# Kernel tuning notes

Measured on AMD Instinct MI355X. Metric: run time of the kernel, lower is better.

Reference implementation:

```python
import jax, jax.numpy as jnp
import numpy as np
import math

VOCAB = 50257
BLOCK = 2048
NE = 768


def setup_inputs() -> dict:
    key = jax.random.key(0)
    ks = jax.random.split(key, 12)
    s = 0.02
    idx = jax.random.randint(ks[0], (4, 2048), 0, VOCAB, dtype=jnp.int64 if jax.config.jax_enable_x64 else jnp.int32)
    tok_emb = jax.random.normal(ks[1], (VOCAB, NE), jnp.float32) * s
    pos_emb = jax.random.normal(ks[2], (BLOCK, NE), jnp.float32) * s
    Wk = jax.random.normal(ks[3], (NE, NE), jnp.float32) * s
    bk = jnp.zeros((NE,), jnp.float32)
    Wq = jax.random.normal(ks[4], (NE, NE), jnp.float32) * s
    bq = jnp.zeros((NE,), jnp.float32)
    Wv = jax.random.normal(ks[5], (NE, NE), jnp.float32) * s
    bv = jnp.zeros((NE,), jnp.float32)
    ln_g = jnp.ones((NE,), jnp.float32)
    ln_b = jnp.zeros((NE,), jnp.float32)
    Wh = jax.random.normal(ks[6], (NE, VOCAB), jnp.float32) * s
    bh = jnp.zeros((VOCAB,), jnp.float32)
    return {"idx": idx, "tok_emb": tok_emb, "pos_emb": pos_emb, "Wq": Wq, "bq": bq,
            "Wk": Wk, "bk": bk, "Wv": Wv, "bv": bv, "ln_g": ln_g, "ln_b": ln_b,
            "Wh": Wh, "bh": bh}


def reference(idx, tok_emb, pos_emb, Wq, bq, Wk, bk, Wv, bv, ln_g, ln_b, Wh, bh):
    B, T = idx.shape
    C = tok_emb.shape[1]
    x = tok_emb[idx] + pos_emb[:T]  # [B,T,C]
    q = jnp.einsum('btc,cd->btd', x, Wq) + bq
    k = jnp.einsum('btc,cd->btd', x, Wk) + bk
    v = jnp.einsum('btc,cd->btd', x, Wv) + bv
    att = jnp.einsum('btd,bsd->bts', q, k) / math.sqrt(C)  # [B,T,T]
    causal = jnp.tril(jnp.ones((T, T), bool))
    att = jnp.where(causal, att, -jnp.inf)
    att = jax.nn.softmax(att, axis=-1)
    y = jnp.einsum('bts,bsd->btd', att, v)
    # LayerNorm (eps=1e-5, torch default)
    mu = jnp.mean(y, axis=-1, keepdims=True)
    var = jnp.mean((y - mu) ** 2, axis=-1, keepdims=True)
    yn = (y - mu) * jax.lax.rsqrt(var + 1e-5) * ln_g + ln_b
    logits = jnp.einsum('btc,cv->btv', yn, Wh) + bh
    return logits
```

## Files before the change

### kernel.cpp

```cpp
#include <hip/hip_runtime.h>
#include <hip/hip_bf16.h>
#include <math.h>

typedef __bf16 bf16x8 __attribute__((ext_vector_type(8)));
typedef float  f32x4  __attribute__((ext_vector_type(4)));

#define GAS(p) ((const __attribute__((address_space(1))) void*)(p))
#define LAS(p) ((__attribute__((address_space(3))) void*)(p))

static constexpr int NE = 768;

__global__ __launch_bounds__(256) void k_embed(const int* __restrict__ idx,
    const float* __restrict__ tok, const float* __restrict__ pos,
    __hip_bfloat16* __restrict__ xb)
{
    int bt = blockIdx.x;
    int t  = bt & 2047;
    int token = idx[bt];
    const float* te = tok + (size_t)token * NE;
    const float* pe = pos + (size_t)t * NE;
    __hip_bfloat16* o = xb + (size_t)bt * NE;
    for (int c = threadIdx.x; c < NE; c += 256)
        o[c] = __float2bfloat16(te[c] + pe[c]);
}

__global__ __launch_bounds__(256) void k_transpose_f32_bf16(
    const float* __restrict__ in, __hip_bfloat16* __restrict__ out,
    int R, int C, int outRows)
{
    __shared__ float tile[32][33];
    int c0 = blockIdx.x * 32, r0 = blockIdx.y * 32;
    int tx = threadIdx.x & 31, ty = threadIdx.x >> 5;
    #pragma unroll
    for (int i = 0; i < 32; i += 8) {
        int r = r0 + ty + i, c = c0 + tx;
        tile[ty + i][tx] = (r < R && c < C) ? in[(size_t)r * C + c] : 0.f;
    }
    __syncthreads();
    #pragma unroll
    for (int i = 0; i < 32; i += 8) {
        int oc = c0 + ty + i, orr = r0 + tx;
        if (oc < outRows && orr < R)
            out[(size_t)oc * R + orr] = __float2bfloat16(tile[tx][ty + i]);
    }
}

__global__ __launch_bounds__(256) void k_transpose_bf16(
    const __hip_bfloat16* __restrict__ in, __hip_bfloat16* __restrict__ out,
    int R, int C)
{
    __shared__ __hip_bfloat16 tile[32][33];
    size_t boff = (size_t)blockIdx.z * R * C;
    int c0 = blockIdx.x * 32, r0 = blockIdx.y * 32;
    int tx = threadIdx.x & 31, ty = threadIdx.x >> 5;
    #pragma unroll
    for (int i = 0; i < 32; i += 8)
        tile[ty + i][tx] = in[boff + (size_t)(r0 + ty + i) * C + (c0 + tx)];
    __syncthreads();
    #pragma unroll
    for (int i = 0; i < 32; i += 8)
        out[boff + (size_t)(c0 + ty + i) * R + (r0 + tx)] = tile[tx][ty + i];
}

__global__ __launch_bounds__(256) void k_pack_bias(const float* __restrict__ bq,
    const float* __restrict__ bk, const float* __restrict__ bv, float* __restrict__ o)
{
    int i = blockIdx.x * 256 + threadIdx.x;
    if (i < 768) o[i] = bq[i];
    else if (i < 1536) o[i] = bk[i - 768];
    else if (i < 2304) o[i] = bv[i - 1536];
}

template<int MODE>
__global__ __launch_bounds__(256) void k_gemm(
    const __hip_bfloat16* __restrict__ A, const __hip_bfloat16* __restrict__ Bt,
    int K, int lda, int ldb,
    size_t strideA, size_t strideB, size_t strideC,
    float* __restrict__ outf, int ldc, int ncols,
    const float* __restrict__ bias, float scale,
    __hip_bfloat16* __restrict__ oq, __hip_bfloat16* __restrict__ ok,
    __hip_bfloat16* __restrict__ ov)
{
    int bn = blockIdx.x, bm = blockIdx.y, bz = blockIdx.z;
    if constexpr (MODE == 2) bm = (int)gridDim.y - 1 - bm;
    if (MODE == 1 && bn > bm) return;
    __shared__ __align__(16) __hip_bfloat16 As[128 * 32];
    __shared__ __align__(16) __hip_bfloat16 Bs[128 * 32];
    const __hip_bfloat16* Ab = A  + bz * strideA + (size_t)bm * 128 * lda;
    const __hip_bfloat16* Bb = Bt + bz * strideB + (size_t)bn * 128 * ldb;
    int tid = threadIdx.x, w = tid >> 6, lane = tid & 63;
    int wr = w >> 1, wc = w & 1;
    f32x4 acc[4][4] = {};
    int sr = tid >> 2, sc = (tid & 3) * 8;
    int lr = lane & 15, lk = (lane >> 4) * 8;

    const int kend = (MODE == 2) ? (bm + 1) * 128 : K;

    for (int k0 = 0; k0 < kend; k0 += 32) {
        __syncthreads();
        #pragma unroll
        for (int i = 0; i < 2; ++i) {
            __builtin_amdgcn_global_load_lds(GAS(Ab + (size_t)(i * 64 + sr) * lda + k0 + sc),
                                             LAS((char*)As + i * 4096 + w * 1024), 16, 0, 0);
            __builtin_amdgcn_global_load_lds(GAS(Bb + (size_t)(i * 64 + sr) * ldb + k0 + sc),
                                             LAS((char*)Bs + i * 4096 + w * 1024), 16, 0, 0);
        }
        __syncthreads();
        bf16x8 af[4], bfv[4];
        #pragma unroll
        for (int mi = 0; mi < 4; ++mi)
            af[mi] = *(const bf16x8*)(As + (wr * 64 + mi * 16 + lr) * 32 + lk);
        #pragma unroll
        for (int ni = 0; ni < 4; ++ni)
            bfv[ni] = *(const bf16x8*)(Bs + (wc * 64 + ni * 16 + lr) * 32 + lk);
        #pragma unroll
        for (int mi = 0; mi < 4; ++mi)
            #pragma unroll
            for (int ni = 0; ni < 4; ++ni)
                acc[mi][ni] = __builtin_amdgcn_mfma_f32_16x16x32_bf16(af[mi], bfv[ni], acc[mi][ni], 0, 0, 0);
    }

    int r4 = (lane >> 4) * 4;
    #pragma unroll
    for (int mi = 0; mi < 4; ++mi) {
        #pragma unroll
        for (int ni = 0; ni < 4; ++ni) {
            #pragma unroll
            for (int r = 0; r < 4; ++r) {
                int row = bm * 128 + wr * 64 + mi * 16 + r4 + r;
                int col = bn * 128 + wc * 64 + ni * 16 + lr;
                float v = acc[mi][ni][r];
                if constexpr (MODE == 0) {
                    v += bias[col];
                    __hip_bfloat16 h = __float2bfloat16(v);
                    if (col < 768)       oq[(size_t)row * 768 + col]          = h;
                    else if (col < 1536) ok[(size_t)row * 768 + (col - 768)]  = h;
                    else                 ov[(size_t)row * 768 + (col - 1536)] = h;
                } else if constexpr (MODE == 1) {
                    outf[bz * strideC + (size_t)row * ldc + col] = v * scale;
                } else {
                    outf[bz * strideC + (size_t)row * ldc + col] = v;
                }
            }
        }
    }
}

__global__ __launch_bounds__(512, 4) void k_gemm_head(
    const __hip_bfloat16* __restrict__ A,
    const __hip_bfloat16* __restrict__ Bt,
    float* __restrict__ out, const float* __restrict__ bias, int ldc, int ncols)
{
    constexpr int K = 768, NT = K / 32;
    __shared__ __align__(16) __hip_bfloat16 As[2][256 * 32];
    __shared__ __align__(16) __hip_bfloat16 Bs[2][128 * 32];

    const int bm = blockIdx.x, bn = blockIdx.y;
    const int tid = threadIdx.x;
    const int w = tid >> 6, lane = tid & 63;
    const int wr = w >> 1, wc = w & 1;
    const int lr = lane & 15, lu = lane >> 4;

    const __hip_bfloat16* Ap = A  + (size_t)(bm * 256) * K;
    const __hip_bfloat16* Bp = Bt + (size_t)(bn * 128) * K;

    f32x4 acc[4][4] = {};

    auto stage = [&](int kt, int pb) {
        #pragma unroll
        for (int l = 0; l < 2; ++l) {
            int v = l * 512 + tid;
            int row = v >> 2, uc = v & 3;
            int s = (row >> 1) & 3;
            __builtin_amdgcn_global_load_lds(GAS(Ap + (size_t)row * K + kt * 32 + ((uc ^ s) << 3)),
                                             LAS(&As[pb][v * 8]), 16, 0, 0);
        }
        {
            int v = tid;
            int row = v >> 2, uc = v & 3;
            int s = (row >> 1) & 3;
            __builtin_amdgcn_global_load_lds(GAS(Bp + (size_t)row * K + kt * 32 + ((uc ^ s) << 3)),
                                             LAS(&Bs[pb][v * 8]), 16, 0, 0);
        }
    };
    auto rdA = [&](int pb, int m) {
        int row = wr * 64 + m * 16 + lr;
        int s = (row >> 1) & 3;
        return *(const bf16x8*)&As[pb][row * 32 + ((lu ^ s) << 3)];
    };
    auto rdB = [&](int pb, int n) {
        int row = wc * 64 + n * 16 + lr;
        int s = (row >> 1) & 3;
        return *(const bf16x8*)&Bs[pb][row * 32 + ((lu ^ s) << 3)];
    };

    stage(0, 0);
    __syncthreads();

    for (int kt = 0; kt < NT; ++kt) {
        const int p = kt & 1;
        if (kt + 1 < NT) stage(kt + 1, p ^ 1);
        bf16x8 bfv[4];
        #pragma unroll
        for (int n = 0; n < 4; ++n) bfv[n] = rdB(p, n);
        #pragma unroll
        for (int m = 0; m < 4; ++m) {
            bf16x8 a = rdA(p, m);
            #pragma unroll
            for (int n = 0; n < 4; ++n)
                acc[m][n] = __builtin_amdgcn_mfma_f32_16x16x32_bf16(a, bfv[n], acc[m][n], 0, 0, 0);
        }
        __syncthreads();
    }

    const int r4 = lu * 4;
    #pragma unroll
    for (int m = 0; m < 4; ++m) {
        #pragma unroll
        for (int n = 0; n < 4; ++n) {
            int col = bn * 128 + wc * 64 + n * 16 + lr;
            if (col < ncols) {
                float bv_ = bias[col];
                #pragma unroll
                for (int r = 0; r < 4; ++r) {
                    int row = bm * 256 + wr * 64 + m * 16 + r4 + r;
                    out[(size_t)row * ldc + col] = acc[m][n][r] + bv_;
                }
            }
        }
    }
}

__global__ __launch_bounds__(256) void k_softmax(const float* __restrict__ att,
    __hip_bfloat16* __restrict__ P, int T)
{
    int t = blockIdx.x, b = blockIdx.y;
    const float* row = att + ((size_t)b * T + t) * T;
    __hip_bfloat16* prow = P + ((size_t)b * T + t) * T;
    const int n = t + 1;
    const int nz = ((t >> 7) + 1) << 7;
    __shared__ float red[256];
    float4 v[2];
    float mx = -1e30f;
    #pragma unroll
    for (int j = 0; j < 2; ++j) {
        int e = (threadIdx.x + j * 256) * 4;
        v[j] = *(const float4*)(row + e);
        #pragma unroll
        for (int k = 0; k < 4; ++k)
            if (e + k < n) mx = fmaxf(mx, ((const float*)&v[j])[k]);
    }
    red[threadIdx.x] = mx; __syncthreads();
    for (int o = 128; o > 0; o >>= 1) {
        if (threadIdx.x < o) red[threadIdx.x] = fmaxf(red[threadIdx.x], red[threadIdx.x + o]);
        __syncthreads();
    }
    mx = red[0]; __syncthreads();
    float ev[8];
    float sum = 0.f;
    #pragma unroll
    for (int j = 0; j < 2; ++j) {
        int e = (threadIdx.x + j * 256) * 4;
        #pragma unroll
        for (int k = 0; k < 4; ++k) {
            float x = ((const float*)&v[j])[k];
            float ex = (e + k < n) ? __expf(x - mx) : 0.f;
            ev[j * 4 + k] = ex;
            sum += ex;
        }
    }
    red[threadIdx.x] = sum; __syncthreads();
    for (int o = 128; o > 0; o >>= 1) {
        if (threadIdx.x < o) red[threadIdx.x] += red[threadIdx.x + o];
        __syncthreads();
    }
    float inv = 1.f / red[0];
    #pragma unroll
    for (int j = 0; j < 2; ++j) {
        int e = (threadIdx.x + j * 256) * 4;
        #pragma unroll
        for (int k = 0; k < 4; ++k)
            if (e + k < nz) prow[e + k] = __float2bfloat16(ev[j * 4 + k] * inv);
    }
}

__global__ __launch_bounds__(256) void k_layernorm(const float* __restrict__ y,
    const float* __restrict__ g, const float* __restrict__ b,
    __hip_bfloat16* __restrict__ yn)
{
    int row = blockIdx.x;
    const float* yr = y + (size_t)row * NE;
    float s = 0.f, s2 = 0.f;
    for (int c = threadIdx.x; c < NE; c += 256) { float v = yr[c]; s += v; s2 += v * v; }
    __shared__ float r1[256], r2[256];
    r1[threadIdx.x] = s; r2[threadIdx.x] = s2; __syncthreads();
    for (int o = 128; o > 0; o >>= 1) {
        if (threadIdx.x < o) { r1[threadIdx.x] += r1[threadIdx.x + o]; r2[threadIdx.x] += r2[threadIdx.x + o]; }
        __syncthreads();
    }
    float mu = r1[0] / NE;
    float var = r2[0] / NE - mu * mu;
    float rs = rsqrtf(var + 1e-5f);
    __hip_bfloat16* o = yn + (size_t)row * NE;
    for (int c = threadIdx.x; c < NE; c += 256)
        o[c] = __float2bfloat16((yr[c] - mu) * rs * g[c] + b[c]);
}

extern "C" void kernel_launch(void* const* d_in, const int* in_sizes, int n_in,
                              void* d_out, int out_size, void* d_ws, size_t ws_size,
                              hipStream_t stream)
{
    const int*   idx  = (const int*)  d_in[0];
    const float* tok  = (const float*)d_in[1];
    const float* pos  = (const float*)d_in[2];
    const float* Wq   = (const float*)d_in[3];
    const float* bq   = (const float*)d_in[4];
    const float* Wk   = (const float*)d_in[5];
    const float* bk   = (const float*)d_in[6];
    const float* Wv   = (const float*)d_in[7];
    const float* bv   = (const float*)d_in[8];
    const float* ln_g = (const float*)d_in[9];
    const float* ln_b = (const float*)d_in[10];
    const float* Wh   = (const float*)d_in[11];
    const float* bh   = (const float*)d_in[12];
    float* out = (float*)d_out;

    const int B = 4, T = 2048, C = 768, V = 50257, Vp = 50432;

    char* p = (char*)d_ws;
    auto take = [&](size_t bytes) { char* r = p; p += (bytes + 255) & ~(size_t)255; return r; };
    __hip_bfloat16* xb    = (__hip_bfloat16*)take((size_t)B * T * C * 2);
    __hip_bfloat16* wqkvT = (__hip_bfloat16*)take((size_t)3 * C * C * 2);
    float*          bqkv  = (float*)take((size_t)3 * C * 4);
    __hip_bfloat16* qb    = (__hip_bfloat16*)take((size_t)B * T * C * 2);
    __hip_bfloat16* kb    = (__hip_bfloat16*)take((size_t)B * T * C * 2);
    __hip_bfloat16* vb    = (__hip_bfloat16*)take((size_t)B * T * C * 2);
    __hip_bfloat16* vT    = (__hip_bfloat16*)take((size_t)B * T * C * 2);
    float*          att   = (float*)take((size_t)B * T * T * 4);
    __hip_bfloat16* P     = (__hip_bfloat16*)take((size_t)B * T * T * 2);
    float*          y     = (float*)take((size_t)B * T * C * 4);
    __hip_bfloat16* yn    = (__hip_bfloat16*)take((size_t)B * T * C * 2);
    __hip_bfloat16* whT   = (__hip_bfloat16*)att;

    float scale = 1.0f / sqrtf((float)C);

    k_embed<<<dim3(B * T), 256, 0, stream>>>(idx, tok, pos, xb);
    k_transpose_f32_bf16<<<dim3(24, 24), 256, 0, stream>>>(Wq, wqkvT,             C, C, C);
    k_transpose_f32_bf16<<<dim3(24, 24), 256, 0, stream>>>(Wk, wqkvT + C * C,     C, C, C);
    k_transpose_f32_bf16<<<dim3(24, 24), 256, 0, stream>>>(Wv, wqkvT + 2 * C * C, C, C, C);
    k_pack_bias<<<dim3(9), 256, 0, stream>>>(bq, bk, bv, bqkv);

    k_gemm<0><<<dim3(18, 64, 1), 256, 0, stream>>>(xb, wqkvT, C, C, C, 0, 0, 0,
        nullptr, 0, 0, bqkv, 1.f, qb, kb, vb);

    k_transpose_bf16<<<dim3(24, 64, B), 256, 0, stream>>>(vb, vT, T, C);

    k_gemm<1><<<dim3(16, 16, B), 256, 0, stream>>>(qb, kb, C, C, C,
        (size_t)T * C, (size_t)T * C, (size_t)T * T, att, T, 0, nullptr, scale,
        nullptr, nullptr, nullptr);

    k_softmax<<<dim3(T, B), 256, 0, stream>>>(att, P, T);

    k_gemm<2><<<dim3(6, 16, B), 256, 0, stream>>>(P, vT, T, T, T,
        (size_t)T * T, (size_t)C * T, (size_t)T * C, y, C, 0, nullptr, 1.f,
        nullptr, nullptr, nullptr);

    k_transpose_f32_bf16<<<dim3(Vp / 32, 24), 256, 0, stream>>>(Wh, whT, C, V, Vp);

    k_layernorm<<<dim3(B * T), 256, 0, stream>>>(y, ln_g, ln_b, yn);

    k_gemm_head<<<dim3(32, Vp / 128), 512, 0, stream>>>(yn, whT, out, bh, V, V);
}
```

Before: 1.361 ms.

## Restructure head GEMM to 128x128 tiles with K=64 stages and prefetch depth two

The vocab-projection GEMM moves from 256x128 tiles with 512 threads and K-step 32 to 128x128 tiles with 256 threads and K-step 64, using an 8-way XOR swizzle in LDS. Two stages are preloaded, and explicit vmcnt/lgkmcnt waits and raw barriers let the next tile's global-to-LDS loads overlap the MFMA work. s_setprio raises wave priority around the MFMA block. The intent is to hide load latency and cut barrier count per FLOP, at the cost of twice as many blocks and less A-tile reuse.

```diff
diff --git a/kernel.cpp b/kernel.cpp
--- a/kernel.cpp
+++ b/kernel.cpp
@@ -146,14 +146,14 @@
     }
 }
 
-__global__ __launch_bounds__(512, 4) void k_gemm_head(
+__global__ __launch_bounds__(256, 2) void k_gemm_head(
     const __hip_bfloat16* __restrict__ A,
     const __hip_bfloat16* __restrict__ Bt,
     float* __restrict__ out, const float* __restrict__ bias, int ldc, int ncols)
 {
-    constexpr int K = 768, NT = K / 32;
-    __shared__ __align__(16) __hip_bfloat16 As[2][256 * 32];
-    __shared__ __align__(16) __hip_bfloat16 Bs[2][128 * 32];
+    constexpr int K = 768, NT = K / 64;
+    __shared__ __align__(16) __hip_bfloat16 As[2][128 * 64];
+    __shared__ __align__(16) __hip_bfloat16 Bs[2][128 * 64];
 
     const int bm = blockIdx.x, bn = blockIdx.y;
     const int tid = threadIdx.x;
@@ -161,56 +161,71 @@
     const int wr = w >> 1, wc = w & 1;
     const int lr = lane & 15, lu = lane >> 4;
 
-    const __hip_bfloat16* Ap = A  + (size_t)(bm * 256) * K;
+    const int sr = tid >> 3;
+    const int su = (tid & 7) ^ (sr & 7);
+    const __hip_bfloat16* Ap = A  + (size_t)(bm * 128) * K;
     const __hip_bfloat16* Bp = Bt + (size_t)(bn * 128) * K;
 
     f32x4 acc[4][4] = {};
 
     auto stage = [&](int kt, int pb) {
         #pragma unroll
-        for (int l = 0; l < 2; ++l) {
-            int v = l * 512 + tid;
-            int row = v >> 2, uc = v & 3;
-            int s = (row >> 1) & 3;
-            __builtin_amdgcn_global_load_lds(GAS(Ap + (size_t)row * K + kt * 32 + ((uc ^ s) << 3)),
+        for (int l = 0; l < 4; ++l) {
+            int v = l * 256 + tid;
+            int row = v >> 3, u = (v & 7) ^ (row & 7);
+            __builtin_amdgcn_global_load_lds(GAS(Ap + (size_t)row * K + kt * 64 + u * 8),
                                              LAS(&As[pb][v * 8]), 16, 0, 0);
         }
-        {
-            int v = tid;
-            int row = v >> 2, uc = v & 3;
-            int s = (row >> 1) & 3;
-            __builtin_amdgcn_global_load_lds(GAS(Bp + (size_t)row * K + kt * 32 + ((uc ^ s) << 3)),
+        #pragma unroll
+        for (int l = 0; l < 4; ++l) {
+            int v = l * 256 + tid;
+            int row = v >> 3, u = (v & 7) ^ (row & 7);
+            __builtin_amdgcn_global_load_lds(GAS(Bp + (size_t)row * K + kt * 64 + u * 8),
                                              LAS(&Bs[pb][v * 8]), 16, 0, 0);
         }
     };
-    auto rdA = [&](int pb, int m) {
+    auto rdA = [&](int pb, int m, int kk) {
         int row = wr * 64 + m * 16 + lr;
-        int s = (row >> 1) & 3;
-        return *(const bf16x8*)&As[pb][row * 32 + ((lu ^ s) << 3)];
+        return *(const bf16x8*)&As[pb][row * 64 + (((kk * 4 + lu) ^ (row & 7)) << 3)];
     };
-    auto rdB = [&](int pb, int n) {
+    auto rdB = [&](int pb, int n, int kk) {
         int row = wc * 64 + n * 16 + lr;
-        int s = (row >> 1) & 3;
-        return *(const bf16x8*)&Bs[pb][row * 32 + ((lu ^ s) << 3)];
+        return *(const bf16x8*)&Bs[pb][row * 64 + (((kk * 4 + lu) ^ (row & 7)) << 3)];
     };
 
     stage(0, 0);
-    __syncthreads();
+    stage(1, 1);
+    asm volatile("s_waitcnt vmcnt(8)" ::: "memory");
+    asm volatile("s_barrier" ::: "memory");
 
     for (int kt = 0; kt < NT; ++kt) {
         const int p = kt & 1;
-        if (kt + 1 < NT) stage(kt + 1, p ^ 1);
-        bf16x8 bfv[4];
-        #pragma unroll
-        for (int n = 0; n < 4; ++n) bfv[n] = rdB(p, n);
-        #pragma unroll
-        for (int m = 0; m < 4; ++m) {
-            bf16x8 a = rdA(p, m);
+        bf16x8 af[4][2], bfv[4][2];
+        #pragma unroll
+        for (int m = 0; m < 4; ++m) { af[m][0] = rdA(p, m, 0); af[m][1] = rdA(p, m, 1); }
+        #pragma unroll
+        for (int n = 0; n < 4; ++n) { bfv[n][0] = rdB(p, n, 0); bfv[n][1] = rdB(p, n, 1); }
+        asm volatile("s_waitcnt lgkmcnt(0)" ::: "memory");
+        asm volatile("s_barrier" ::: "memory");
+        if (kt + 2 < NT) {
+            stage(kt + 2, p);
+            asm volatile("s_waitcnt vmcnt(8)" ::: "memory");
+        } else if (kt + 1 < NT) {
+            asm volatile("s_waitcnt vmcnt(0)" ::: "memory");
+        }
+        asm volatile("s_barrier" ::: "memory");
+        __builtin_amdgcn_s_setprio(1);
+        #pragma unroll
+        for (int m = 0; m < 4; ++m)
             #pragma unroll
             for (int n = 0; n < 4; ++n)
-                acc[m][n] = __builtin_amdgcn_mfma_f32_16x16x32_bf16(a, bfv[n], acc[m][n], 0, 0, 0);
-        }
-        __syncthreads();
+                acc[m][n] = __builtin_amdgcn_mfma_f32_16x16x32_bf16(af[m][0], bfv[n][0], acc[m][n], 0, 0, 0);
+        #pragma unroll
+        for (int m = 0; m < 4; ++m)
+            #pragma unroll
+            for (int n = 0; n < 4; ++n)
+                acc[m][n] = __builtin_amdgcn_mfma_f32_16x16x32_bf16(af[m][1], bfv[n][1], acc[m][n], 0, 0, 0);
+        __builtin_amdgcn_s_setprio(0);
     }
 
     const int r4 = lu * 4;
@@ -223,7 +238,7 @@
                 float bv_ = bias[col];
                 #pragma unroll
                 for (int r = 0; r < 4; ++r) {
-                    int row = bm * 256 + wr * 64 + m * 16 + r4 + r;
+                    int row = bm * 128 + wr * 64 + m * 16 + r4 + r;
                     out[(size_t)row * ldc + col] = acc[m][n][r] + bv_;
                 }
             }
@@ -369,5 +384,5 @@
 
     k_layernorm<<<dim3(B * T), 256, 0, stream>>>(y, ln_g, ln_b, yn);
 
-    k_gemm_head<<<dim3(32, Vp / 128), 512, 0, stream>>>(yn, whT, out, bh, V, V);
-}
+    k_gemm_head<<<dim3(64, Vp / 128), 256, 0, stream>>>(yn, whT, out, bh, V, V);
+}
```

Result: slower. 1.644 ms (+20.8%).
